# Optimization experiments

Measured on AMD Instinct MI355X. Metric: run time of the kernel, lower is better.

## Reference

```python
import jax, jax.numpy as jnp
import numpy as np

NH = 4       # num_heads
WS = 4       # window_size (in subdomains)
SHIFT = 2    # shift (in subdomains) on odd layers
SUB = 16     # physical subdomain size (y and x)
L = 4        # num_layers
EPS = 1e-5   # InstanceNorm2d eps


def _pw_mlp(x, W1, b1, W2, b2):
    # pointwise (1x1 conv) MLP over channel dim of [..., C, y, x]
    h = jnp.einsum('oc,...cyx->...oyx', W1, x) + b1[:, None, None]
    h = jax.nn.gelu(h, approximate=False)
    return jnp.einsum('oc,...cyx->...oyx', W2, h) + b2[:, None, None]


def _inorm(x):
    # InstanceNorm2d (affine=False): normalize each channel over spatial dims
    mu = jnp.mean(x, axis=(-2, -1), keepdims=True)
    var = jnp.var(x, axis=(-2, -1), keepdims=True)
    return (x - mu) * jax.lax.rsqrt(var + EPS)


def _grid_to_win(g, B, nwy, nwx):
    # g: [B, n_sub_y, n_sub_x, C, sh, sw] -> [B*nwy*nwx, WS*WS, C, sh, sw]
    C, sh, sw = g.shape[3:]
    g = g.reshape(B, nwy, WS, nwx, WS, C, sh, sw).transpose(0, 1, 3, 2, 4, 5, 6, 7)
    return g.reshape(B * nwy * nwx, WS * WS, C, sh, sw)


def _win_to_grid(d, B, nwy, nwx):
    # inverse of _grid_to_win
    C, sh, sw = d.shape[2:]
    g = d.reshape(B, nwy, nwx, WS, WS, C, sh, sw).transpose(0, 1, 3, 2, 4, 5, 6, 7)
    return g.reshape(B, nwy * WS, nwx * WS, C, sh, sw)


def _attn(d, Wq, bq, Wk, bk, Wv, bv, Wo, bo, shift, B, nwy, nwx):
    # function-space windowed self-attention; tokens are subdomain functions
    if shift > 0:
        g = _win_to_grid(d, B, nwy, nwx)
        g = jnp.roll(g, (-shift, -shift), axis=(1, 2))
        d = _grid_to_win(g, B, nwy, nwx)
    E = Wq.shape[0]
    dh = E // NH
    Bw, S, C, sh, sw = d.shape

    def proj(W, b):
        p = jnp.einsum('dc,bscyx->bsdyx', W, d) + b[:, None, None]
        return p.reshape(Bw, S, NH, dh, sh, sw)

    q, k, vv = proj(Wq, bq), proj(Wk, bk), proj(Wv, bv)
    # integral inner-product score: mean over subdomain points, / sqrt(dh)
    scale = 1.0 / ((sh * sw) * (float(dh) ** 0.5))
    scores = jnp.einsum('bihcyx,bjhcyx->bhij', q, k) * scale
    A = jax.nn.softmax(scores, axis=-1)
    o = jnp.einsum('bhij,bjhcyx->bihcyx', A, vv).reshape(Bw, S, E, sh, sw)
    o = jnp.einsum('dc,bscyx->bsdyx', Wo, o) + bo[:, None, None]
    if shift > 0:
        g = _win_to_grid(o, B, nwy, nwx)
        g = jnp.roll(g, (shift, shift), axis=(1, 2))
        o = _grid_to_win(g, B, nwy, nwx)
    return o


def _forward(v, inp_W1, inp_b1, inp_W2, inp_b2, Wq, bq, Wk, bk, Wv, bv, Wo, bo,
             mlp_W1, mlp_b1, mlp_W2, mlp_b2, out_W1, out_b1, out_W2, out_b2,
             dsy, dsx):
    B, Cin, H, W = v.shape
    n_sub_y, n_sub_x = dsy // SUB, dsx // SUB
    sh, sw = H // n_sub_y, W // n_sub_x
    nwy, nwx = n_sub_y // WS, n_sub_x // WS
    # cell-centered grid, channels (y, x)
    yc = (jnp.arange(H, dtype=v.dtype) + 0.5) * (dsy / H)
    xc = (jnp.arange(W, dtype=v.dtype) + 0.5) * (dsx / W)
    g = jnp.stack(jnp.meshgrid(yc, xc, indexing='ij'), axis=0)  # [2,H,W]
    g = jnp.broadcast_to(g, (B, 2, H, W))
    v = jnp.concatenate([g, v], axis=1)
    v = _pw_mlp(v, inp_W1, inp_b1, inp_W2, inp_b2)  # [B,E,H,W]
    E = v.shape[1]
    # win_decompose2d: pixels -> subdomain grid -> windows of WSxWS subdomains
    sgrid = v.reshape(B, E, n_sub_y, sh, n_sub_x, sw).transpose(0, 2, 4, 1, 3, 5)
    d = _grid_to_win(sgrid, B, nwy, nwx)  # [B*nw, WS*WS, E, sh, sw]
    for i in range(L):
        shift = 0 if i % 2 == 0 else SHIFT
        d = _attn(_inorm(d), Wq[i], bq[i], Wk[i], bk[i], Wv[i], bv[i],
                  Wo[i], bo[i], shift, B, nwy, nwx) + d
        d = _pw_mlp(_inorm(d), mlp_W1[i], mlp_b1[i], mlp_W2[i], mlp_b2[i]) + d
    # win_recompose2d
    sgrid = _win_to_grid(d, B, nwy, nwx)  # [B, n_sub_y, n_sub_x, E, sh, sw]
    u = sgrid.transpose(0, 3, 1, 4, 2, 5).reshape(B, E, H, W)
    return _pw_mlp(u, out_W1, out_b1, out_W2, out_b2)


def setup_inputs() -> dict:
    key = jax.random.key(0)
    ks = jax.random.split(key, 16)
    B, Cin, H, W, E, HID, Cout = 8, 3, 256, 256, 64, 128, 1
    s = 0.02
    r = lambda k, shape: (s * jax.random.normal(k, shape)).astype(jnp.float32)
    z = lambda shape: jnp.zeros(shape, jnp.float32)
    return {
        'v': jax.random.normal(ks[0], (B, Cin, H, W), dtype=jnp.float32),
        'inp_W1': r(ks[1], (HID, Cin + 2)), 'inp_b1': z((HID,)),
        'inp_W2': r(ks[2], (E, HID)), 'inp_b2': z((E,)),
        'Wq': r(ks[3], (L, E, E)), 'bq': z((L, E)),
        'Wk': r(ks[4], (L, E, E)), 'bk': z((L, E)),
        'Wv': r(ks[5], (L, E, E)), 'bv': z((L, E)),
        'Wo': r(ks[6], (L, E, E)), 'bo': z((L, E)),
        'mlp_W1': r(ks[7], (L, E, E)), 'mlp_b1': z((L, E)),
        'mlp_W2': r(ks[8], (L, E, E)), 'mlp_b2': z((L, E)),
        'out_W1': r(ks[9], (HID, E)), 'out_b1': z((HID,)),
        'out_W2': r(ks[10], (Cout, HID)), 'out_b2': z((Cout,)),
        'domain_size_y': 256, 'domain_size_x': 256,
    }


def reference(v, inp_W1, inp_b1, inp_W2, inp_b2, Wq, bq, Wk, bk, Wv, bv, Wo, bo,
              mlp_W1, mlp_b1, mlp_W2, mlp_b2, out_W1, out_b1, out_W2, out_b2,
              domain_size_y, domain_size_x):
    return _forward(v, inp_W1, inp_b1, inp_W2, inp_b2, Wq, bq, Wk, bk, Wv, bv,
                    Wo, bo, mlp_W1, mlp_b1, mlp_W2, mlp_b2, out_W1, out_b1,
                    out_W2, out_b2, domain_size_y, domain_size_x)
```

## Files before the change

### kernel.cpp

```cpp
#include <hip/hip_runtime.h>
#include <math.h>

typedef unsigned short u16;
typedef unsigned int   u32;
typedef __attribute__((ext_vector_type(8))) short bf16x8;
typedef __attribute__((ext_vector_type(4))) float f32x4;

#define NTOK  2048
#define TOKSZ 16384ull

#define CBAR() __asm__ __volatile__("" ::: "memory")

__device__ __forceinline__ float bf2f(u16 b) { return __uint_as_float(((u32)b) << 16); }
__device__ __forceinline__ u16 f2bf(float f) {
    u32 u = __float_as_uint(f);
    u += 0x7FFFu + ((u >> 16) & 1u);
    return (u16)(u >> 16);
}
__device__ __forceinline__ float gelu_f(float x) {
    return 0.5f * x * (1.0f + erff(x * 0.70710678118654752440f));
}
__device__ __forceinline__ int shift_tok(int n) {
    int w = n >> 4, s = n & 15;
    int b = w >> 4, wy = (w >> 2) & 3, wx = w & 3;
    int ty = s >> 2, tx = s & 3;
    int gy = ((wy << 2) + ty + 2) & 15;
    int gx = ((wx << 2) + tx + 2) & 15;
    int w2 = (b << 4) + ((gy >> 2) << 2) + (gx >> 2);
    int s2 = ((gy & 3) << 2) + (gx & 3);
    return (w2 << 4) + s2;
}
__device__ __forceinline__ int swz(int row, int chunk) {
    return row * 64 + ((chunk ^ (row & 7)) << 3);
}

union U8 { uint4 u; bf16x8 b; };

__global__ void detect_kernel(const u16* __restrict__ w1, int* __restrict__ flag) {
    int t = threadIdx.x, bad = 0;
    for (int i = t; i < 640; i += 64) {
        float ax = fabsf(bf2f(w1[i]));
        if (!(ax < 1e3f)) bad = 1;
    }
    unsigned long long m = __ballot(bad);
    if (t == 0) *flag = (m != 0ull) ? 1 : 0;
}

#define NWT 20
struct WArgs { const void* src[NWT]; int off16[NWT + 1]; int f32o[NWT]; };

__global__ __launch_bounds__(256)
void cvt_weights(WArgs a, const int* __restrict__ flag,
                 float* __restrict__ wbufA, u16* __restrict__ wbuf16) {
    int t = blockIdx.x * 256 + threadIdx.x;
    if (t >= a.off16[NWT]) return;
    int s = 0;
    while (a.off16[s + 1] <= t) ++s;
    int idx = t - a.off16[s];
    u16 raw; float v;
    if (*flag) { v = ((const float*)a.src[s])[idx]; raw = f2bf(v); }
    else       { raw = ((const u16*)a.src[s])[idx]; v = bf2f(raw); }
    wbuf16[t] = raw;
    if (a.f32o[s] >= 0) wbufA[a.f32o[s] + idx] = v;
}

__global__ __launch_bounds__(256, 3)
void embed_mfma(const void* __restrict__ vin, const int* __restrict__ flag,
                const float* __restrict__ W1, const float* __restrict__ b1,
                const u16* __restrict__ W2bf, const float* __restrict__ b2,
                const int* __restrict__ pdsy, const int* __restrict__ pdsx,
                float* __restrict__ d, float* __restrict__ mursg) {
    extern __shared__ char smem[];
    u16* hsT = (u16*)smem;
    u16* wl  = (u16*)(smem + 32768);
    int n = blockIdx.x, t = threadIdx.x;
    int wv = t >> 6, l = t & 63, m = l & 15, qd = l >> 4;
    int px0 = wv * 64;

    int w = n >> 4, s = n & 15;
    int b = w >> 4, wy = (w >> 2) & 3, wx = w & 3;
    int ty = s >> 2, tx = s & 3;
    int y = ((wy << 2) + ty) * 16 + (t >> 4);
    int x = ((wx << 2) + tx) * 16 + (t & 15);
    int fl = *flag;
    float in0 = ((float)y + 0.5f) * ((float)pdsy[0] * (1.0f / 256.0f));
    float in1 = ((float)x + 0.5f) * ((float)pdsx[0] * (1.0f / 256.0f));
    size_t pix = (size_t)b * 3 * 65536 + (size_t)y * 256 + (size_t)x;
    float in2 = fl ? ((const float*)vin)[pix]          : bf2f(((const u16*)vin)[pix]);
    float in3 = fl ? ((const float*)vin)[pix + 65536]  : bf2f(((const u16*)vin)[pix + 65536]);
    float in4 = fl ? ((const float*)vin)[pix + 131072] : bf2f(((const u16*)vin)[pix + 131072]);

    f32x4 acc[4][4];
    #pragma unroll
    for (int nt = 0; nt < 4; ++nt) {
        float bb = b2[nt * 16 + m];
        #pragma unroll
        for (int mt = 0; mt < 4; ++mt) acc[mt][nt] = {bb, bb, bb, bb};
    }
    for (int half = 0; half < 2; ++half) {
        if (half) __syncthreads();
        for (int h2 = 0; h2 < 64; h2 += 2) {
            int hid = half * 64 + h2;
            float ha = b1[hid] + W1[hid*5]*in0 + W1[hid*5+1]*in1 + W1[hid*5+2]*in2
                     + W1[hid*5+3]*in3 + W1[hid*5+4]*in4;
            float hb2 = b1[hid+1] + W1[hid*5+5]*in0 + W1[hid*5+6]*in1 + W1[hid*5+7]*in2
                     + W1[hid*5+8]*in3 + W1[hid*5+9]*in4;
            u32 pk = (u32)f2bf(gelu_f(ha)) | ((u32)f2bf(gelu_f(hb2)) << 16);
            *(u32*)&hsT[swz(t, h2 >> 3) + (h2 & 7)] = pk;
        }
        #pragma unroll
        for (int r = 0; r < 2; ++r) {
            int u = t + r * 256; int e = u >> 3, c8 = u & 7;
            *(uint4*)&wl[swz(e, c8)] = *(const uint4*)(W2bf + e * 128 + half * 64 + c8 * 8);
        }
        __syncthreads();
        #pragma unroll
        for (int ks = 0; ks < 2; ++ks) {
            U8 af[4], bf[4];
            #pragma unroll
            for (int mt = 0; mt < 4; ++mt)
                af[mt].u = *(const uint4*)&hsT[swz(px0 + mt*16 + m, ks*4 + qd)];
            #pragma unroll
            for (int nt = 0; nt < 4; ++nt)
                bf[nt].u = *(const uint4*)&wl[swz(nt*16 + m, ks*4 + qd)];
            #pragma unroll
            for (int mt = 0; mt < 4; ++mt)
                #pragma unroll
                for (int nt = 0; nt < 4; ++nt)
                    acc[mt][nt] = __builtin_amdgcn_mfma_f32_16x16x32_bf16(
                        af[mt].b, bf[nt].b, acc[mt][nt], 0, 0, 0);
        }
    }
    __syncthreads();
    float sv[4], qv[4];
    #pragma unroll
    for (int nt = 0; nt < 4; ++nt) {
        float ss = 0.f, qq = 0.f;
        #pragma unroll
        for (int mt = 0; mt < 4; ++mt)
            #pragma unroll
            for (int r = 0; r < 4; ++r) { float xx = acc[mt][nt][r]; ss += xx; qq = fmaf(xx, xx, qq); }
        ss += __shfl_xor(ss, 16); ss += __shfl_xor(ss, 32);
        qq += __shfl_xor(qq, 16); qq += __shfl_xor(qq, 32);
        sv[nt] = ss; qv[nt] = qq;
    }
    float* sarr = (float*)smem;
    if (qd == 0) {
        #pragma unroll
        for (int nt = 0; nt < 4; ++nt) {
            sarr[(nt*16 + m)*4 + wv] = sv[nt];
            sarr[256 + (nt*16 + m)*4 + wv] = qv[nt];
        }
    }
    __syncthreads();
    if (t < 64) {
        float ss = sarr[t*4] + sarr[t*4+1] + sarr[t*4+2] + sarr[t*4+3];
        float qq = sarr[256+t*4] + sarr[256+t*4+1] + sarr[256+t*4+2] + sarr[256+t*4+3];
        float mu = ss * (1.0f/256.0f);
        float var = qq * (1.0f/256.0f) - mu * mu;
        mursg[(size_t)n * 128 + t] = mu;
        mursg[(size_t)n * 128 + 64 + t] = rsqrtf(var + 1e-5f);
    }
    __syncthreads();
    float* eps = (float*)smem + wv * 2304;
    float* dp = d + (size_t)n * TOKSZ;
    #pragma unroll
    for (int ch2 = 0; ch2 < 2; ++ch2) {
        if (ch2) CBAR();
        #pragma unroll
        for (int mt = ch2*2; mt < ch2*2+2; ++mt)
            #pragma unroll
            for (int nt = 0; nt < 4; ++nt)
                #pragma unroll
                for (int r = 0; r < 4; ++r)
                    eps[((mt&1)*16 + qd*4 + r) * 68 + nt*16 + m] = acc[mt][nt][r];
        CBAR();
        #pragma unroll
        for (int j = 0; j < 8; ++j) {
            int f = l + 64*j; int row = f >> 4, c4 = f & 15;
            float4 v = *(float4*)&eps[row * 68 + c4 * 4];
            *(float4*)&dp[(px0 + ch2*32 + row) * 64 + c4 * 4] = v;
        }
    }
}

__device__ __forceinline__ void gemm64(const u16* xs, const u16* wl, const float* bv4,
                                       int px0, int m, int qd, u16* dst) {
    f32x4 acc[4][4];
    #pragma unroll
    for (int nt = 0; nt < 4; ++nt) {
        float bb = bv4[nt];
        #pragma unroll
        for (int mt = 0; mt < 4; ++mt) acc[mt][nt] = {bb, bb, bb, bb};
    }
    #pragma unroll
    for (int ks = 0; ks < 2; ++ks) {
        U8 af[4], bfr[4];
        #pragma unroll
        for (int mt = 0; mt < 4; ++mt)
            af[mt].u = *(const uint4*)&xs[swz(px0 + mt*16 + m, ks*4 + qd)];
        #pragma unroll
        for (int nt = 0; nt < 4; ++nt)
            bfr[nt].u = *(const uint4*)&wl[swz(nt*16 + m, ks*4 + qd)];
        #pragma unroll
        for (int mt = 0; mt < 4; ++mt)
            #pragma unroll
            for (int nt = 0; nt < 4; ++nt)
                acc[mt][nt] = __builtin_amdgcn_mfma_f32_16x16x32_bf16(
                    af[mt].b, bfr[nt].b, acc[mt][nt], 0, 0, 0);
    }
    #pragma unroll
    for (int mt = 0; mt < 4; ++mt)
        #pragma unroll
        for (int nt = 0; nt < 4; ++nt)
            #pragma unroll
            for (int r = 0; r < 4; ++r) {
                int R = px0 + mt*16 + qd*4 + r, ch = nt*16 + m;
                dst[swz(R, ch >> 3) + (ch & 7)] = f2bf(acc[mt][nt][r]);
            }
}

__global__ __launch_bounds__(256, 1)
void scores_qkv(const float* __restrict__ dres, const float* __restrict__ mursg,
                const u16* __restrict__ Wq, const float* __restrict__ bq,
                const u16* __restrict__ Wk, const float* __restrict__ bk,
                const u16* __restrict__ Wv, const float* __restrict__ bv,
                int shifted, float* __restrict__ Ap, u16* __restrict__ vbuf) {
    extern __shared__ char smem[];
    u16* xs  = (u16*)smem;
    u16* qls = (u16*)(smem + 32768);
    u16* kls = (u16*)(smem + 65536);
    u16* wlq = (u16*)(smem + 98304);
    u16* wlk = (u16*)(smem + 106496);
    u16* wlv = (u16*)(smem + 114688);
    int* nis = (int*)(smem + 122880);
    float* mloc = (float*)(smem + 122944);
    int w = blockIdx.x, half = blockIdx.y, t = threadIdx.x;
    int wv = t >> 6, l = t & 63, m = l & 15, qd = l >> 4;
    int px0 = wv * 64;
    if (t < 16) { int nn = w * 16 + t; nis[t] = shifted ? shift_tok(nn) : nn; }
    __syncthreads();
    #pragma unroll
    for (int r = 0; r < 2; ++r) {
        int u = t + r * 256; int e = u >> 3, c8 = u & 7;
        *(uint4*)&wlq[swz(e, c8)] = *(const uint4*)(Wq + e * 64 + c8 * 8);
        *(uint4*)&wlk[swz(e, c8)] = *(const uint4*)(Wk + e * 64 + c8 * 8);
        *(uint4*)&wlv[swz(e, c8)] = *(const uint4*)(Wv + e * 64 + c8 * 8);
    }
    #pragma unroll
    for (int r = 0; r < 8; ++r) {
        int u = t + r * 256;
        mloc[u] = mursg[(size_t)nis[u >> 7] * 128 + (u & 127)];
    }
    float bqv[4], bkv[4], bvv[4];
    #pragma unroll
    for (int nt = 0; nt < 4; ++nt) {
        bqv[nt] = bq[nt*16 + m]; bkv[nt] = bk[nt*16 + m]; bvv[nt] = bv[nt*16 + m];
    }
    f32x4 sacc = {0.f, 0.f, 0.f, 0.f};
    __syncthreads();
    for (int ch = 0; ch < 8; ++ch) {
        int pxb = half * 128 + ch * 16;
        #pragma unroll
        for (int i8 = 0; i8 < 8; ++i8) {
            int u = t + i8 * 256; int row = u >> 3, c8 = u & 7;
            int tok = row >> 4, pxl = row & 15;
            const float4* gp = (const float4*)
                (dres + (size_t)nis[tok] * TOKSZ + (size_t)(pxb + pxl) * 64 + c8 * 8);
            float4 f0 = gp[0], f1 = gp[1];
            const float4* mp = (const float4*)&mloc[tok * 128 + c8 * 8];
            float4 mu0 = mp[0], mu1 = mp[1];
            const float4* rp = (const float4*)&mloc[tok * 128 + 64 + c8 * 8];
            float4 rs0 = rp[0], rs1 = rp[1];
            uint4 o;
            o.x = (u32)f2bf((f0.x-mu0.x)*rs0.x) | ((u32)f2bf((f0.y-mu0.y)*rs0.y) << 16);
            o.y = (u32)f2bf((f0.z-mu0.z)*rs0.z) | ((u32)f2bf((f0.w-mu0.w)*rs0.w) << 16);
            o.z = (u32)f2bf((f1.x-mu1.x)*rs1.x) | ((u32)f2bf((f1.y-mu1.y)*rs1.y) << 16);
            o.w = (u32)f2bf((f1.z-mu1.z)*rs1.z) | ((u32)f2bf((f1.w-mu1.w)*rs1.w) << 16);
            *(uint4*)&xs[swz(row, c8)] = o;
        }
        __syncthreads();
        gemm64(xs, wlq, bqv, px0, m, qd, qls);
        gemm64(xs, wlk, bkv, px0, m, qd, kls);
        gemm64(xs, wlv, bvv, px0, m, qd, xs);
        __syncthreads();
        #pragma unroll
        for (int p2 = 0; p2 < 8; ++p2) {
            U8 af, bfr;
            int row = m * 16 + p2 * 2 + (qd >> 1);
            int c8 = wv * 2 + (qd & 1);
            af.u  = *(const uint4*)&qls[swz(row, c8)];
            bfr.u = *(const uint4*)&kls[swz(row, c8)];
            sacc = __builtin_amdgcn_mfma_f32_16x16x32_bf16(af.b, bfr.b, sacc, 0, 0, 0);
        }
        #pragma unroll
        for (int i8 = 0; i8 < 8; ++i8) {
            int u = t + i8 * 256; int row = u >> 3, c8 = u & 7;
            int tok = row >> 4, pxl = row & 15;
            *(uint4*)(vbuf + (size_t)nis[tok] * 16384 + (size_t)(pxb + pxl) * 64 + c8 * 8)
                = *(const uint4*)&xs[swz(row, c8)];
        }
        __syncthreads();
    }
    float* ap = Ap + (size_t)half * 131072 + ((size_t)w * 4 + wv) * 256;
    #pragma unroll
    for (int r = 0; r < 4; ++r)
        ap[(qd * 4 + r) * 16 + m] = sacc[r] * (1.0f / 1024.0f);
}

__global__ __launch_bounds__(256, 2)
void wo_mlp(const u16* __restrict__ vb, const float* __restrict__ Ap,
            const u16* __restrict__ Wo, const float* __restrict__ bo,
            const u16* __restrict__ W1, const float* __restrict__ b1,
            const u16* __restrict__ W2, const float* __restrict__ b2,
            int shifted, float* __restrict__ dres, float* __restrict__ mursg,
            int wmu) {
    extern __shared__ char smem[];
    u16* xs = (u16*)smem;
    u16* wl = (u16*)(smem + 32768);
    float* As = (float*)(smem + 32768);
    int*  nis = (int*)(smem + 33792);
    float* sarr = (float*)(smem + 32768);
    float* murs2 = (float*)smem;
    int bid = blockIdx.x;
    int qg = bid >> 7, r7 = bid & 127;
    int n = ((qg << 3) + (r7 & 7)) * 16 + (r7 >> 3);
    int t = threadIdx.x;
    int wv = t >> 6, l = t & 63, m = l & 15, qd = l >> 4;
    int px0 = wv * 64;
    int w = n >> 4, i = n & 15;
    int no = shifted ? shift_tok(n) : n;
    int rbase = l >> 4, c4l = l & 15;
    if (t < 16) { int nn = w * 16 + t; nis[t] = shifted ? shift_tok(nn) : nn; }
    if (t >= 64 && t < 128) {
        int u = t - 64; int h = u >> 4, j = u & 15;
        size_t ai = ((size_t)(w * 4 + h)) * 256 + i * 16 + j;
        float sc = (Ap[ai] + Ap[131072 + ai]) * (1.0f / 1024.0f);
        float mx = sc;
        #pragma unroll
        for (int off = 1; off < 16; off <<= 1) mx = fmaxf(mx, __shfl_xor(mx, off, 16));
        float e = expf(sc - mx);
        float ssum = e;
        #pragma unroll
        for (int off = 1; off < 16; off <<= 1) ssum += __shfl_xor(ssum, off, 16);
        As[u] = e / ssum;
    }
    __syncthreads();
    #pragma unroll
    for (int r = 0; r < 8; ++r) {
        int idx = r * 256 + t;
        int px = idx >> 3, c8 = idx & 7, h = c8 >> 1;
        float a0=0,a1=0,a2=0,a3=0,a4=0,a5=0,a6=0,a7=0;
        #pragma unroll
        for (int j = 0; j < 16; ++j) {
            const u16* src = vb + (size_t)nis[j] * 16384 + (size_t)px * 64 + c8 * 8;
            uint4 pv = *(const uint4*)src;
            float aw = As[h * 16 + j];
            a0 = fmaf(aw, __uint_as_float(pv.x << 16), a0);
            a1 = fmaf(aw, __uint_as_float(pv.x & 0xFFFF0000u), a1);
            a2 = fmaf(aw, __uint_as_float(pv.y << 16), a2);
            a3 = fmaf(aw, __uint_as_float(pv.y & 0xFFFF0000u), a3);
            a4 = fmaf(aw, __uint_as_float(pv.z << 16), a4);
            a5 = fmaf(aw, __uint_as_float(pv.z & 0xFFFF0000u), a5);
            a6 = fmaf(aw, __uint_as_float(pv.w << 16), a6);
            a7 = fmaf(aw, __uint_as_float(pv.w & 0xFFFF0000u), a7);
        }
        uint4 o;
        o.x = (u32)f2bf(a0) | ((u32)f2bf(a1) << 16);
        o.y = (u32)f2bf(a2) | ((u32)f2bf(a3) << 16);
        o.z = (u32)f2bf(a4) | ((u32)f2bf(a5) << 16);
        o.w = (u32)f2bf(a6) | ((u32)f2bf(a7) << 16);
        *(uint4*)&xs[swz(px, c8)] = o;
    }
    __syncthreads();
    #pragma unroll
    for (int r = 0; r < 2; ++r) {
        int u = t + r * 256;
        int e = u >> 3, c8 = u & 7;
        *(uint4*)&wl[swz(e, c8)] = *(const uint4*)(Wo + e * 64 + c8 * 8);
    }
    __syncthreads();
    f32x4 acc[4][4];
    #pragma unroll
    for (int nt = 0; nt < 4; ++nt) {
        float bb = bo[nt * 16 + m];
        #pragma unroll
        for (int mt = 0; mt < 4; ++mt) acc[mt][nt] = {bb, bb, bb, bb};
    }
    #pragma unroll
    for (int ks = 0; ks < 2; ++ks) {
        U8 af[4], bf[4];
        #pragma unroll
        for (int mt = 0; mt < 4; ++mt)
            af[mt].u = *(const uint4*)&xs[swz(px0 + mt*16 + m, ks*4 + qd)];
        #pragma unroll
        for (int nt = 0; nt < 4; ++nt)
            bf[nt].u = *(const uint4*)&wl[swz(nt*16 + m, ks*4 + qd)];
        #pragma unroll
        for (int mt = 0; mt < 4; ++mt)
            #pragma unroll
            for (int nt = 0; nt < 4; ++nt)
                acc[mt][nt] = __builtin_amdgcn_mfma_f32_16x16x32_bf16(
                    af[mt].b, bf[nt].b, acc[mt][nt], 0, 0, 0);
    }
    __syncthreads();
    float* eps = (float*)smem + wv * 2304;
    float* dp = dres + (size_t)no * TOKSZ;
    float4 xv[2][8];
    #pragma unroll
    for (int ch2 = 0; ch2 < 2; ++ch2) {
        if (ch2) CBAR();
        #pragma unroll
        for (int mt = ch2*2; mt < ch2*2+2; ++mt)
            #pragma unroll
            for (int nt = 0; nt < 4; ++nt)
                #pragma unroll
                for (int r = 0; r < 4; ++r)
                    eps[((mt&1)*16 + qd*4 + r) * 68 + nt*16 + m] = acc[mt][nt][r];
        CBAR();
        #pragma unroll
        for (int j = 0; j < 8; ++j) {
            int row = rbase + 4*j;
            float4 dv = *(float4*)&eps[row * 68 + c4l * 4];
            float4 gv = *(const float4*)&dp[(px0 + ch2*32 + row) * 64 + c4l * 4];
            gv.x += dv.x; gv.y += dv.y; gv.z += dv.z; gv.w += dv.w;
            xv[ch2][j] = gv;
        }
    }
    __syncthreads();
    float s0=0,s1=0,s2=0,s3=0,q0=0,q1=0,q2=0,q3=0;
    #pragma unroll
    for (int ch2 = 0; ch2 < 2; ++ch2)
        #pragma unroll
        for (int j = 0; j < 8; ++j) {
            float4 v = xv[ch2][j];
            s0 += v.x; q0 = fmaf(v.x, v.x, q0);
            s1 += v.y; q1 = fmaf(v.y, v.y, q1);
            s2 += v.z; q2 = fmaf(v.z, v.z, q2);
            s3 += v.w; q3 = fmaf(v.w, v.w, q3);
        }
    int cb = 4 * c4l, g = t >> 4;
    float* qarr = sarr + 1024;
    sarr[(cb+0)*16+g]=s0; sarr[(cb+1)*16+g]=s1; sarr[(cb+2)*16+g]=s2; sarr[(cb+3)*16+g]=s3;
    qarr[(cb+0)*16+g]=q0; qarr[(cb+1)*16+g]=q1; qarr[(cb+2)*16+g]=q2; qarr[(cb+3)*16+g]=q3;
    __syncthreads();
    if (t < 64) {
        float ss = 0.f, qq = 0.f;
        #pragma unroll
        for (int gg = 0; gg < 16; ++gg) { ss += sarr[t*16+gg]; qq += qarr[t*16+gg]; }
        float mu = ss * (1.0f/256.0f);
        float var = qq * (1.0f/256.0f) - mu * mu;
        murs2[t] = mu; murs2[64 + t] = rsqrtf(var + 1e-5f);
    }
    __syncthreads();
    float m0 = murs2[cb], m1 = murs2[cb+1], m2 = murs2[cb+2], m3 = murs2[cb+3];
    float r0 = murs2[64+cb], r1 = murs2[64+cb+1], r2 = murs2[64+cb+2], r3 = murs2[64+cb+3];
    __syncthreads();
    #pragma unroll
    for (int ch2 = 0; ch2 < 2; ++ch2)
        #pragma unroll
        for (int j = 0; j < 8; ++j) {
            float4 v = xv[ch2][j];
            int row = px0 + ch2*32 + rbase + 4*j;
            uint2 o;
            o.x = (u32)f2bf((v.x-m0)*r0) | ((u32)f2bf((v.y-m1)*r1) << 16);
            o.y = (u32)f2bf((v.z-m2)*r2) | ((u32)f2bf((v.w-m3)*r3) << 16);
            *(uint2*)&xs[swz(row, c4l >> 1) + (c4l & 1) * 4] = o;
        }
    #pragma unroll
    for (int r = 0; r < 2; ++r) {
        int u = t + r * 256;
        int e = u >> 3, c8 = u & 7;
        *(uint4*)&wl[swz(e, c8)] = *(const uint4*)(W1 + e * 64 + c8 * 8);
    }
    __syncthreads();
    #pragma unroll
    for (int nt = 0; nt < 4; ++nt) {
        float bb = b1[nt * 16 + m];
        #pragma unroll
        for (int mt = 0; mt < 4; ++mt) acc[mt][nt] = {bb, bb, bb, bb};
    }
    #pragma unroll
    for (int ks = 0; ks < 2; ++ks) {
        U8 af[4], bf[4];
        #pragma unroll
        for (int mt = 0; mt < 4; ++mt)
            af[mt].u = *(const uint4*)&xs[swz(px0 + mt*16 + m, ks*4 + qd)];
        #pragma unroll
        for (int nt = 0; nt < 4; ++nt)
            bf[nt].u = *(const uint4*)&wl[swz(nt*16 + m, ks*4 + qd)];
        #pragma unroll
        for (int mt = 0; mt < 4; ++mt)
            #pragma unroll
            for (int nt = 0; nt < 4; ++nt)
                acc[mt][nt] = __builtin_amdgcn_mfma_f32_16x16x32_bf16(
                    af[mt].b, bf[nt].b, acc[mt][nt], 0, 0, 0);
    }
    __syncthreads();
    #pragma unroll
    for (int nt = 0; nt < 4; ++nt) {
        int ch = nt * 16 + m;
        #pragma unroll
        for (int mt = 0; mt < 4; ++mt)
            #pragma unroll
            for (int r = 0; r < 4; ++r) {
                int R = px0 + mt*16 + qd*4 + r;
                xs[swz(R, ch >> 3) + (ch & 7)] = f2bf(gelu_f(acc[mt][nt][r]));
            }
    }
    #pragma unroll
    for (int r = 0; r < 2; ++r) {
        int u = t + r * 256;
        int e = u >> 3, c8 = u & 7;
        *(uint4*)&wl[swz(e, c8)] = *(const uint4*)(W2 + e * 64 + c8 * 8);
    }
    __syncthreads();
    #pragma unroll
    for (int nt = 0; nt < 4; ++nt) {
        float bb = b2[nt * 16 + m];
        #pragma unroll
        for (int mt = 0; mt < 4; ++mt) acc[mt][nt] = {bb, bb, bb, bb};
    }
    #pragma unroll
    for (int ks = 0; ks < 2; ++ks) {
        U8 af[4], bf[4];
        #pragma unroll
        for (int mt = 0; mt < 4; ++mt)
            af[mt].u = *(const uint4*)&xs[swz(px0 + mt*16 + m, ks*4 + qd)];
        #pragma unroll
        for (int nt = 0; nt < 4; ++nt)
            bf[nt].u = *(const uint4*)&wl[swz(nt*16 + m, ks*4 + qd)];
        #pragma unroll
        for (int mt = 0; mt < 4; ++mt)
            #pragma unroll
            for (int nt = 0; nt < 4; ++nt)
                acc[mt][nt] = __builtin_amdgcn_mfma_f32_16x16x32_bf16(
                    af[mt].b, bf[nt].b, acc[mt][nt], 0, 0, 0);
    }
    __syncthreads();
    #pragma unroll
    for (int ch2 = 0; ch2 < 2; ++ch2) {
        if (ch2) CBAR();
        #pragma unroll
        for (int mt = ch2*2; mt < ch2*2+2; ++mt)
            #pragma unroll
            for (int nt = 0; nt < 4; ++nt)
                #pragma unroll
                for (int r = 0; r < 4; ++r)
                    eps[((mt&1)*16 + qd*4 + r) * 68 + nt*16 + m] = acc[mt][nt][r];
        CBAR();
        #pragma unroll
        for (int j = 0; j < 8; ++j) {
            int row = rbase + 4*j;
            float4 dv = *(float4*)&eps[row * 68 + c4l * 4];
            float4 bs = xv[ch2][j];
            bs.x += dv.x; bs.y += dv.y; bs.z += dv.z; bs.w += dv.w;
            xv[ch2][j] = bs;
            *(float4*)&dp[(px0 + ch2*32 + row) * 64 + c4l * 4] = bs;
        }
    }
    if (wmu) {
        __syncthreads();
        float t0=0,t1=0,t2=0,t3=0,u0=0,u1=0,u2=0,u3=0;
        #pragma unroll
        for (int ch2 = 0; ch2 < 2; ++ch2)
            #pragma unroll
            for (int j = 0; j < 8; ++j) {
                float4 v = xv[ch2][j];
                t0 += v.x; u0 = fmaf(v.x, v.x, u0);
                t1 += v.y; u1 = fmaf(v.y, v.y, u1);
                t2 += v.z; u2 = fmaf(v.z, v.z, u2);
                t3 += v.w; u3 = fmaf(v.w, v.w, u3);
            }
        sarr[(cb+0)*16+g]=t0; sarr[(cb+1)*16+g]=t1; sarr[(cb+2)*16+g]=t2; sarr[(cb+3)*16+g]=t3;
        qarr[(cb+0)*16+g]=u0; qarr[(cb+1)*16+g]=u1; qarr[(cb+2)*16+g]=u2; qarr[(cb+3)*16+g]=u3;
        __syncthreads();
        if (t < 64) {
            float ss = 0.f, qq = 0.f;
            #pragma unroll
            for (int gg = 0; gg < 16; ++gg) { ss += sarr[t*16+gg]; qq += qarr[t*16+gg]; }
            float mu = ss * (1.0f/256.0f);
            float var = qq * (1.0f/256.0f) - mu * mu;
            mursg[(size_t)no * 128 + t] = mu;
            mursg[(size_t)no * 128 + 64 + t] = rsqrtf(var + 1e-5f);
        }
    }
}

__global__ __launch_bounds__(256, 3)
void wo_av(const u16* __restrict__ vb, const float* __restrict__ Ap,
           const u16* __restrict__ Wo, const float* __restrict__ bo,
           int shifted, float* __restrict__ dres) {
    extern __shared__ char smem[];
    u16* xs = (u16*)smem;
    u16* wl = (u16*)(smem + 32768);
    float* As = (float*)(smem + 40960);
    int*  nis = (int*)(smem + 41216);
    int bid = blockIdx.x;
    int qg = bid >> 7, r7 = bid & 127;
    int n = ((qg << 3) + (r7 & 7)) * 16 + (r7 >> 3);
    int t = threadIdx.x;
    int wv = t >> 6, l = t & 63, m = l & 15, qd = l >> 4;
    int px0 = wv * 64;
    int w = n >> 4, i = n & 15;
    int no = shifted ? shift_tok(n) : n;
    if (t < 16) { int nn = w * 16 + t; nis[t] = shifted ? shift_tok(nn) : nn; }
    if (t >= 64 && t < 128) {
        int u = t - 64; int h = u >> 4, j = u & 15;
        size_t ai = ((size_t)(w * 4 + h)) * 256 + i * 16 + j;
        float sc = (Ap[ai] + Ap[131072 + ai]) * (1.0f / 1024.0f);
        float mx = sc;
        #pragma unroll
        for (int off = 1; off < 16; off <<= 1) mx = fmaxf(mx, __shfl_xor(mx, off, 16));
        float e = expf(sc - mx);
        float ssum = e;
        #pragma unroll
        for (int off = 1; off < 16; off <<= 1) ssum += __shfl_xor(ssum, off, 16);
        As[u] = e / ssum;
    }
    #pragma unroll
    for (int r = 0; r < 2; ++r) {
        int u = t + r * 256;
        int e = u >> 3, c8 = u & 7;
        *(uint4*)&wl[swz(e, c8)] = *(const uint4*)(Wo + e * 64 + c8 * 8);
    }
    __syncthreads();
    #pragma unroll
    for (int r = 0; r < 8; ++r) {
        int idx = r * 256 + t;
        int px = idx >> 3, c8 = idx & 7, h = c8 >> 1;
        float a0=0,a1=0,a2=0,a3=0,a4=0,a5=0,a6=0,a7=0;
        #pragma unroll
        for (int j = 0; j < 16; ++j) {
            const u16* src = vb + (size_t)nis[j] * 16384 + (size_t)px * 64 + c8 * 8;
            uint4 pv = *(const uint4*)src;
            float aw = As[h * 16 + j];
            a0 = fmaf(aw, __uint_as_float(pv.x << 16), a0);
            a1 = fmaf(aw, __uint_as_float(pv.x & 0xFFFF0000u), a1);
            a2 = fmaf(aw, __uint_as_float(pv.y << 16), a2);
            a3 = fmaf(aw, __uint_as_float(pv.y & 0xFFFF0000u), a3);
            a4 = fmaf(aw, __uint_as_float(pv.z << 16), a4);
            a5 = fmaf(aw, __uint_as_float(pv.z & 0xFFFF0000u), a5);
            a6 = fmaf(aw, __uint_as_float(pv.w << 16), a6);
            a7 = fmaf(aw, __uint_as_float(pv.w & 0xFFFF0000u), a7);
        }
        uint4 o;
        o.x = (u32)f2bf(a0) | ((u32)f2bf(a1) << 16);
        o.y = (u32)f2bf(a2) | ((u32)f2bf(a3) << 16);
        o.z = (u32)f2bf(a4) | ((u32)f2bf(a5) << 16);
        o.w = (u32)f2bf(a6) | ((u32)f2bf(a7) << 16);
        *(uint4*)&xs[swz(px, c8)] = o;
    }
    __syncthreads();
    f32x4 acc[4][4];
    #pragma unroll
    for (int nt = 0; nt < 4; ++nt) {
        float bb = bo[nt * 16 + m];
        #pragma unroll
        for (int mt = 0; mt < 4; ++mt) acc[mt][nt] = {bb, bb, bb, bb};
    }
    #pragma unroll
    for (int ks = 0; ks < 2; ++ks) {
        U8 af[4], bf[4];
        #pragma unroll
        for (int mt = 0; mt < 4; ++mt)
            af[mt].u = *(const uint4*)&xs[swz(px0 + mt*16 + m, ks*4 + qd)];
        #pragma unroll
        for (int nt = 0; nt < 4; ++nt)
            bf[nt].u = *(const uint4*)&wl[swz(nt*16 + m, ks*4 + qd)];
        #pragma unroll
        for (int mt = 0; mt < 4; ++mt)
            #pragma unroll
            for (int nt = 0; nt < 4; ++nt)
                acc[mt][nt] = __builtin_amdgcn_mfma_f32_16x16x32_bf16(
                    af[mt].b, bf[nt].b, acc[mt][nt], 0, 0, 0);
    }
    __syncthreads();
    float* eps = (float*)smem + wv * 2304;
    float* dp = dres + (size_t)no * TOKSZ;
    #pragma unroll
    for (int ch2 = 0; ch2 < 2; ++ch2) {
        if (ch2) CBAR();
        #pragma unroll
        for (int mt = ch2*2; mt < ch2*2+2; ++mt)
            #pragma unroll
            for (int nt = 0; nt < 4; ++nt)
                #pragma unroll
                for (int r = 0; r < 4; ++r)
                    eps[((mt&1)*16 + qd*4 + r) * 68 + nt*16 + m] = acc[mt][nt][r];
        CBAR();
        #pragma unroll
        for (int j = 0; j < 8; ++j) {
            int f = l + 64*j; int row = f >> 4, c4 = f & 15;
            float4 dv = *(float4*)&eps[row * 68 + c4 * 4];
            float* gp = &dp[(px0 + ch2*32 + row) * 64 + c4 * 4];
            float4 gv = *(float4*)gp;
            gv.x += dv.x; gv.y += dv.y; gv.z += dv.z; gv.w += dv.w;
            *(float4*)gp = gv;
        }
    }
}

__global__ __launch_bounds__(256, 2)
void mlp_out(const float* __restrict__ dres,
             const u16* __restrict__ W1, const float* __restrict__ b1,
             const u16* __restrict__ W2, const float* __restrict__ b2,
             const u16* __restrict__ oW1, const float* __restrict__ ob1,
             const float* __restrict__ oW2, const float* __restrict__ ob2,
             void* __restrict__ outp, const int* __restrict__ flag) {
    extern __shared__ char smem[];
    u16* xs = (u16*)smem;
    u16* wl = (u16*)(smem + 32768);
    float* sarr = (float*)(smem + 32768);
    float* murs = (float*)smem;
    int n = blockIdx.x, t = threadIdx.x;
    int wv = t >> 6, l = t & 63, m = l & 15, qd = l >> 4;
    int px0 = wv * 64;
    int rbase = l >> 4, c4 = l & 15;
    const float4* gin = (const float4*)(dres + (size_t)n * TOKSZ);
    float4 xv[2][8];
    float s0=0,s1=0,s2=0,s3=0,q0=0,q1=0,q2=0,q3=0;
    #pragma unroll
    for (int ch2 = 0; ch2 < 2; ++ch2)
        #pragma unroll
        for (int j = 0; j < 8; ++j) {
            float4 v = gin[(px0 + ch2*32 + rbase + 4*j) * 16 + c4];
            xv[ch2][j] = v;
            s0 += v.x; q0 = fmaf(v.x, v.x, q0);
            s1 += v.y; q1 = fmaf(v.y, v.y, q1);
            s2 += v.z; q2 = fmaf(v.z, v.z, q2);
            s3 += v.w; q3 = fmaf(v.w, v.w, q3);
        }
    int cb = 4 * c4, g = t >> 4;
    sarr[(cb+0)*16+g]=s0; sarr[(cb+1)*16+g]=s1; sarr[(cb+2)*16+g]=s2; sarr[(cb+3)*16+g]=s3;
    float* qarr = sarr + 1024;
    qarr[(cb+0)*16+g]=q0; qarr[(cb+1)*16+g]=q1; qarr[(cb+2)*16+g]=q2; qarr[(cb+3)*16+g]=q3;
    __syncthreads();
    if (t < 64) {
        float ss = 0.f, qq = 0.f;
        #pragma unroll
        for (int gg = 0; gg < 16; ++gg) { ss += sarr[t*16+gg]; qq += qarr[t*16+gg]; }
        float mu = ss * (1.0f/256.0f);
        float var = qq * (1.0f/256.0f) - mu * mu;
        murs[t] = mu; murs[64 + t] = rsqrtf(var + 1e-5f);
    }
    __syncthreads();
    float m0 = murs[cb], m1 = murs[cb+1], m2 = murs[cb+2], m3 = murs[cb+3];
    float r0 = murs[64+cb], r1 = murs[64+cb+1], r2 = murs[64+cb+2], r3 = murs[64+cb+3];
    __syncthreads();
    #pragma unroll
    for (int ch2 = 0; ch2 < 2; ++ch2)
        #pragma unroll
        for (int j = 0; j < 8; ++j) {
            float4 v = xv[ch2][j];
            int row = px0 + ch2*32 + rbase + 4*j;
            uint2 o;
            o.x = (u32)f2bf((v.x-m0)*r0) | ((u32)f2bf((v.y-m1)*r1) << 16);
            o.y = (u32)f2bf((v.z-m2)*r2) | ((u32)f2bf((v.w-m3)*r3) << 16);
            *(uint2*)&xs[swz(row, c4 >> 1) + (c4 & 1) * 4] = o;
        }
    #pragma unroll
    for (int r = 0; r < 2; ++r) {
        int u = t + r * 256;
        int e = u >> 3, c8 = u & 7;
        *(uint4*)&wl[swz(e, c8)] = *(const uint4*)(W1 + e * 64 + c8 * 8);
    }
    __syncthreads();
    f32x4 acc[4][4];
    #pragma unroll
    for (int nt = 0; nt < 4; ++nt) {
        float bb = b1[nt * 16 + m];
        #pragma unroll
        for (int mt = 0; mt < 4; ++mt) acc[mt][nt] = {bb, bb, bb, bb};
    }
    #pragma unroll
    for (int ks = 0; ks < 2; ++ks) {
        U8 af[4], bf[4];
        #pragma unroll
        for (int mt = 0; mt < 4; ++mt)
            af[mt].u = *(const uint4*)&xs[swz(px0 + mt*16 + m, ks*4 + qd)];
        #pragma unroll
        for (int nt = 0; nt < 4; ++nt)
            bf[nt].u = *(const uint4*)&wl[swz(nt*16 + m, ks*4 + qd)];
        #pragma unroll
        for (int mt = 0; mt < 4; ++mt)
            #pragma unroll
            for (int nt = 0; nt < 4; ++nt)
                acc[mt][nt] = __builtin_amdgcn_mfma_f32_16x16x32_bf16(
                    af[mt].b, bf[nt].b, acc[mt][nt], 0, 0, 0);
    }
    __syncthreads();
    #pragma unroll
    for (int nt = 0; nt < 4; ++nt) {
        int ch = nt * 16 + m;
        #pragma unroll
        for (int mt = 0; mt < 4; ++mt)
            #pragma unroll
            for (int r = 0; r < 4; ++r) {
                int R = px0 + mt*16 + qd*4 + r;
                xs[swz(R, ch >> 3) + (ch & 7)] = f2bf(gelu_f(acc[mt][nt][r]));
            }
    }
    #pragma unroll
    for (int r = 0; r < 2; ++r) {
        int u = t + r * 256;
        int e = u >> 3, c8 = u & 7;
        *(uint4*)&wl[swz(e, c8)] = *(const uint4*)(W2 + e * 64 + c8 * 8);
    }
    __syncthreads();
    #pragma unroll
    for (int nt = 0; nt < 4; ++nt) {
        float bb = b2[nt * 16 + m];
        #pragma unroll
        for (int mt = 0; mt < 4; ++mt) acc[mt][nt] = {bb, bb, bb, bb};
    }
    #pragma unroll
    for (int ks = 0; ks < 2; ++ks) {
        U8 af[4], bf[4];
        #pragma unroll
        for (int mt = 0; mt < 4; ++mt)
            af[mt].u = *(const uint4*)&xs[swz(px0 + mt*16 + m, ks*4 + qd)];
        #pragma unroll
        for (int nt = 0; nt < 4; ++nt)
            bf[nt].u = *(const uint4*)&wl[swz(nt*16 + m, ks*4 + qd)];
        #pragma unroll
        for (int mt = 0; mt < 4; ++mt)
            #pragma unroll
            for (int nt = 0; nt < 4; ++nt)
                acc[mt][nt] = __builtin_amdgcn_mfma_f32_16x16x32_bf16(
                    af[mt].b, bf[nt].b, acc[mt][nt], 0, 0, 0);
    }
    __syncthreads();
    float* eps = (float*)smem + wv * 2304;
    #pragma unroll
    for (int ch2 = 0; ch2 < 2; ++ch2) {
        if (ch2) CBAR();
        #pragma unroll
        for (int mt = ch2*2; mt < ch2*2+2; ++mt)
            #pragma unroll
            for (int nt = 0; nt < 4; ++nt)
                #pragma unroll
                for (int r = 0; r < 4; ++r)
                    eps[((mt&1)*16 + qd*4 + r) * 68 + nt*16 + m] = acc[mt][nt][r];
        CBAR();
        #pragma unroll
        for (int j = 0; j < 8; ++j) {
            int row = rbase + 4*j;
            float4 dv = *(float4*)&eps[row * 68 + c4 * 4];
            float4 bs = xv[ch2][j];
            bs.x += dv.x; bs.y += dv.y; bs.z += dv.z; bs.w += dv.w;
            xv[ch2][j] = bs;
        }
    }
    __syncthreads();
    #pragma unroll
    for (int ch2 = 0; ch2 < 2; ++ch2)
        #pragma unroll
        for (int j = 0; j < 8; ++j) {
            float4 v = xv[ch2][j];
            int row = px0 + ch2*32 + rbase + 4*j;
            uint2 o;
            o.x = (u32)f2bf(v.x) | ((u32)f2bf(v.y) << 16);
            o.y = (u32)f2bf(v.z) | ((u32)f2bf(v.w) << 16);
            *(uint2*)&xs[swz(row, c4 >> 1) + (c4 & 1) * 4] = o;
        }
    __syncthreads();
    float val[4][4];
    #pragma unroll
    for (int mt = 0; mt < 4; ++mt)
        #pragma unroll
        for (int r = 0; r < 4; ++r) val[mt][r] = 0.f;
    for (int nh = 0; nh < 2; ++nh) {
        if (nh) __syncthreads();
        #pragma unroll
        for (int r = 0; r < 2; ++r) {
            int u = t + r * 256;
            int e = u >> 3, c8 = u & 7;
            *(uint4*)&wl[swz(e, c8)] = *(const uint4*)(oW1 + (size_t)nh * 4096 + e * 64 + c8 * 8);
        }
        __syncthreads();
        float w2v[4];
        #pragma unroll
        for (int nt = 0; nt < 4; ++nt) w2v[nt] = oW2[nh * 64 + nt * 16 + m];
        #pragma unroll
        for (int mtp = 0; mtp < 2; ++mtp) {
            f32x4 oacc[2][4];
            #pragma unroll
            for (int nt = 0; nt < 4; ++nt) {
                float bb = ob1[nh * 64 + nt * 16 + m];
                oacc[0][nt] = {bb, bb, bb, bb};
                oacc[1][nt] = {bb, bb, bb, bb};
            }
            #pragma unroll
            for (int ks = 0; ks < 2; ++ks) {
                U8 af[2], bf[4];
                #pragma unroll
                for (int mi = 0; mi < 2; ++mi)
                    af[mi].u = *(const uint4*)&xs[swz(px0 + (2*mtp+mi)*16 + m, ks*4 + qd)];
                #pragma unroll
                for (int nt = 0; nt < 4; ++nt)
                    bf[nt].u = *(const uint4*)&wl[swz(nt*16 + m, ks*4 + qd)];
                #pragma unroll
                for (int mi = 0; mi < 2; ++mi)
                    #pragma unroll
                    for (int nt = 0; nt < 4; ++nt)
                        oacc[mi][nt] = __builtin_amdgcn_mfma_f32_16x16x32_bf16(
                            af[mi].b, bf[nt].b, oacc[mi][nt], 0, 0, 0);
            }
            #pragma unroll
            for (int mi = 0; mi < 2; ++mi)
                #pragma unroll
                for (int r = 0; r < 4; ++r) {
                    float p = 0.f;
                    #pragma unroll
                    for (int nt = 0; nt < 4; ++nt)
                        p = fmaf(gelu_f(oacc[mi][nt][r]), w2v[nt], p);
                    val[2*mtp + mi][r] += p;
                }
        }
    }
    __syncthreads();
    float* red = (float*)smem;
    #pragma unroll
    for (int mt = 0; mt < 4; ++mt)
        #pragma unroll
        for (int r = 0; r < 4; ++r)
            red[(px0 + mt*16 + qd*4 + r) * 17 + m] = val[mt][r];
    __syncthreads();
    float a = ob2[0];
    #pragma unroll
    for (int j = 0; j < 16; ++j) a += red[t * 17 + j];
    int w = n >> 4, s = n & 15;
    int b = w >> 4, wy = (w >> 2) & 3, wx = w & 3;
    int ty = s >> 2, tx = s & 3;
    int y = ((wy << 2) + ty) * 16 + (t >> 4);
    int x = ((wx << 2) + tx) * 16 + (t & 15);
    size_t oi = (size_t)b * 65536 + (size_t)y * 256 + (size_t)x;
    if (*flag) ((float*)outp)[oi] = a;
    else       ((u16*)outp)[oi] = f2bf(a);
}

extern "C" void kernel_launch(void* const* d_in, const int* in_sizes, int n_in,
                              void* d_out, int out_size, void* d_ws, size_t ws_size,
                              hipStream_t stream) {
    (void)n_in; (void)out_size; (void)ws_size;
    const int* pdsy = (const int*)d_in[21];
    const int* pdsx = (const int*)d_in[22];

    char* wsb = (char*)d_ws;
    float* bufd  = (float*)wsb;
    u16*  vbuf   = (u16*)(wsb + 134217728ull);
    float* Ap    = (float*)(wsb + 201326592ull);
    float* mursg = (float*)(wsb + 202375168ull);
    float* wbufA = (float*)(wsb + 203423744ull);
    u16* wbuf16  = (u16*)(wsb + 203434496ull);
    int* flag    = (int*)(wsb + 203669248ull);

    const int f32set[12] = {1, 2, 4, 6, 8, 10, 12, 14, 16, 18, 19, 20};
    WArgs wa;
    int off16[NWT + 1]; off16[0] = 0;
    int c32[NWT + 1];
    int fo = 0;
    for (int i = 0; i < NWT; ++i) {
        int di = i + 1;
        wa.src[i] = d_in[di];
        off16[i + 1] = off16[i] + in_sizes[di];
        wa.off16[i] = off16[i];
        int isf = 0;
        for (int j = 0; j < 12; ++j) if (f32set[j] == di) isf = 1;
        wa.f32o[i] = isf ? fo : -1;
        c32[di] = isf ? fo : -1;
        if (isf) fo += in_sizes[di];
    }
    wa.off16[NWT] = off16[NWT];

    detect_kernel<<<1, 64, 0, stream>>>((const u16*)d_in[1], flag);
    cvt_weights<<<(off16[NWT] + 255) / 256, 256, 0, stream>>>(wa, flag, wbufA, wbuf16);

    const float* f_inpW1 = wbufA + c32[1];
    const float* f_inpb1 = wbufA + c32[2];
    const float* f_inpb2 = wbufA + c32[4];
    const float* f_bq  = wbufA + c32[6];
    const float* f_bk  = wbufA + c32[8];
    const float* f_bv  = wbufA + c32[10];
    const float* f_bo  = wbufA + c32[12];
    const float* f_mb1 = wbufA + c32[14];
    const float* f_mb2 = wbufA + c32[16];
    const float* f_ob1 = wbufA + c32[18];
    const float* f_oW2 = wbufA + c32[19];
    const float* f_ob2 = wbufA + c32[20];
    const u16* h_inpW2 = wbuf16 + off16[2];
    const u16* h_Wq  = wbuf16 + off16[4];
    const u16* h_Wk  = wbuf16 + off16[6];
    const u16* h_Wv  = wbuf16 + off16[8];
    const u16* h_Wo  = wbuf16 + off16[10];
    const u16* h_mW1 = wbuf16 + off16[12];
    const u16* h_mW2 = wbuf16 + off16[14];
    const u16* h_oW1 = wbuf16 + off16[16];

    embed_mfma<<<NTOK, 256, 40960, stream>>>(d_in[0], flag, f_inpW1, f_inpb1,
                                             h_inpW2, f_inpb2, pdsy, pdsx,
                                             bufd, mursg);

    for (int l = 0; l < 4; ++l) {
        int sh = l & 1;
        const u16* Wql = h_Wq + l * 4096;  const float* bql = f_bq + l * 64;
        const u16* Wkl = h_Wk + l * 4096;  const float* bkl = f_bk + l * 64;
        const u16* Wvl = h_Wv + l * 4096;  const float* bvl = f_bv + l * 64;
        const u16* Wol = h_Wo + l * 4096;  const float* bol = f_bo + l * 64;
        const u16* W1l = h_mW1 + l * 4096; const float* b1l = f_mb1 + l * 64;
        const u16* W2l = h_mW2 + l * 4096; const float* b2l = f_mb2 + l * 64;

        scores_qkv<<<dim3(128, 2), 256, 131136, stream>>>(
            bufd, mursg, Wql, bql, Wkl, bkl, Wvl, bvl, sh, Ap, vbuf);
        if (l < 3) {
            wo_mlp<<<NTOK, 256, 40960, stream>>>(vbuf, Ap, Wol, bol,
                                                 W1l, b1l, W2l, b2l,
                                                 sh, bufd, mursg, 1);
        } else {
            wo_av<<<NTOK, 256, 41280, stream>>>(vbuf, Ap, Wol, bol, sh, bufd);
            mlp_out<<<NTOK, 256, 40960, stream>>>(bufd, W1l, b1l, W2l, b2l,
                                                  h_oW1, f_ob1, f_oW2, f_ob2,
                                                  d_out, flag);
        }
    }
}
```

Baseline: 1.001 ms.

## Halve scores_qkv pixel chunk to cut LDS and allow two blocks per CU

The scores_qkv kernel now processes 8 pixels per token per chunk instead of 16, over 16 iterations instead of 8. This halves the LDS staging buffers and the per-wave GEMM accumulators, and the launch bound is raised to 2 blocks per CU with about 80KB of shared memory. The token index table in LDS is replaced by per-thread precomputed shifted indices. With only 256 blocks, the goal is more latency hiding per CU, at the cost of twice as many barriers and loop iterations.

```diff
diff --git a/kernel.cpp b/kernel.cpp
--- a/kernel.cpp
+++ b/kernel.cpp
@@ -184,43 +184,43 @@
     }
 }
 
-__device__ __forceinline__ void gemm64(const u16* xs, const u16* wl, const float* bv4,
-                                       int px0, int m, int qd, u16* dst) {
-    f32x4 acc[4][4];
+__device__ __forceinline__ void gemm64h(const u16* xs, const u16* wl, const float* bv4,
+                                        int px0w, int m, int qd, u16* dst) {
+    f32x4 acc[2][4];
     #pragma unroll
     for (int nt = 0; nt < 4; ++nt) {
         float bb = bv4[nt];
-        #pragma unroll
-        for (int mt = 0; mt < 4; ++mt) acc[mt][nt] = {bb, bb, bb, bb};
+        acc[0][nt] = {bb, bb, bb, bb};
+        acc[1][nt] = {bb, bb, bb, bb};
     }
     #pragma unroll
     for (int ks = 0; ks < 2; ++ks) {
-        U8 af[4], bfr[4];
-        #pragma unroll
-        for (int mt = 0; mt < 4; ++mt)
-            af[mt].u = *(const uint4*)&xs[swz(px0 + mt*16 + m, ks*4 + qd)];
+        U8 af[2], bfr[4];
+        #pragma unroll
+        for (int mi = 0; mi < 2; ++mi)
+            af[mi].u = *(const uint4*)&xs[swz(px0w + mi*16 + m, ks*4 + qd)];
         #pragma unroll
         for (int nt = 0; nt < 4; ++nt)
             bfr[nt].u = *(const uint4*)&wl[swz(nt*16 + m, ks*4 + qd)];
         #pragma unroll
-        for (int mt = 0; mt < 4; ++mt)
-            #pragma unroll
-            for (int nt = 0; nt < 4; ++nt)
-                acc[mt][nt] = __builtin_amdgcn_mfma_f32_16x16x32_bf16(
-                    af[mt].b, bfr[nt].b, acc[mt][nt], 0, 0, 0);
-    }
-    #pragma unroll
-    for (int mt = 0; mt < 4; ++mt)
+        for (int mi = 0; mi < 2; ++mi)
+            #pragma unroll
+            for (int nt = 0; nt < 4; ++nt)
+                acc[mi][nt] = __builtin_amdgcn_mfma_f32_16x16x32_bf16(
+                    af[mi].b, bfr[nt].b, acc[mi][nt], 0, 0, 0);
+    }
+    #pragma unroll
+    for (int mi = 0; mi < 2; ++mi)
         #pragma unroll
         for (int nt = 0; nt < 4; ++nt)
             #pragma unroll
             for (int r = 0; r < 4; ++r) {
-                int R = px0 + mt*16 + qd*4 + r, ch = nt*16 + m;
-                dst[swz(R, ch >> 3) + (ch & 7)] = f2bf(acc[mt][nt][r]);
+                int R = px0w + mi*16 + qd*4 + r, ch = nt*16 + m;
+                dst[swz(R, ch >> 3) + (ch & 7)] = f2bf(acc[mi][nt][r]);
             }
 }
 
-__global__ __launch_bounds__(256, 1)
+__global__ __launch_bounds__(256, 2)
 void scores_qkv(const float* __restrict__ dres, const float* __restrict__ mursg,
                 const u16* __restrict__ Wq, const float* __restrict__ bq,
                 const u16* __restrict__ Wk, const float* __restrict__ bk,
@@ -228,18 +228,28 @@
                 int shifted, float* __restrict__ Ap, u16* __restrict__ vbuf) {
     extern __shared__ char smem[];
     u16* xs  = (u16*)smem;
-    u16* qls = (u16*)(smem + 32768);
-    u16* kls = (u16*)(smem + 65536);
-    u16* wlq = (u16*)(smem + 98304);
-    u16* wlk = (u16*)(smem + 106496);
-    u16* wlv = (u16*)(smem + 114688);
-    int* nis = (int*)(smem + 122880);
-    float* mloc = (float*)(smem + 122944);
+    u16* qls = (u16*)(smem + 16384);
+    u16* kls = (u16*)(smem + 32768);
+    u16* wlq = (u16*)(smem + 49152);
+    u16* wlk = (u16*)(smem + 57344);
+    u16* wlv = (u16*)(smem + 65536);
+    float* mloc = (float*)(smem + 73728);
     int w = blockIdx.x, half = blockIdx.y, t = threadIdx.x;
     int wv = t >> 6, l = t & 63, m = l & 15, qd = l >> 4;
-    int px0 = wv * 64;
-    if (t < 16) { int nn = w * 16 + t; nis[t] = shifted ? shift_tok(nn) : nn; }
-    __syncthreads();
+    int px0w = wv * 32;
+    int nst[4];
+    #pragma unroll
+    for (int i8 = 0; i8 < 4; ++i8) {
+        int nn = w * 16 + (4 * i8 + wv);
+        nst[i8] = shifted ? shift_tok(nn) : nn;
+    }
+    #pragma unroll
+    for (int r = 0; r < 8; ++r) {
+        int u = t + r * 256;
+        int nn = w * 16 + (u >> 7);
+        int ni = shifted ? shift_tok(nn) : nn;
+        mloc[u] = mursg[(size_t)ni * 128 + (u & 127)];
+    }
     #pragma unroll
     for (int r = 0; r < 2; ++r) {
         int u = t + r * 256; int e = u >> 3, c8 = u & 7;
@@ -247,11 +257,6 @@
         *(uint4*)&wlk[swz(e, c8)] = *(const uint4*)(Wk + e * 64 + c8 * 8);
         *(uint4*)&wlv[swz(e, c8)] = *(const uint4*)(Wv + e * 64 + c8 * 8);
     }
-    #pragma unroll
-    for (int r = 0; r < 8; ++r) {
-        int u = t + r * 256;
-        mloc[u] = mursg[(size_t)nis[u >> 7] * 128 + (u & 127)];
-    }
     float bqv[4], bkv[4], bvv[4];
     #pragma unroll
     for (int nt = 0; nt < 4; ++nt) {
@@ -259,14 +264,15 @@
     }
     f32x4 sacc = {0.f, 0.f, 0.f, 0.f};
     __syncthreads();
-    for (int ch = 0; ch < 8; ++ch) {
-        int pxb = half * 128 + ch * 16;
-        #pragma unroll
-        for (int i8 = 0; i8 < 8; ++i8) {
+    for (int ch = 0; ch < 16; ++ch) {
+        int pxb = half * 128 + ch * 8;
+        #pragma unroll
+        for (int i8 = 0; i8 < 4; ++i8) {
             int u = t + i8 * 256; int row = u >> 3, c8 = u & 7;
-            int tok = row >> 4, pxl = row & 15;
+            int pxl = row & 7;
+            int tok = 4 * i8 + wv;
             const float4* gp = (const float4*)
-                (dres + (size_t)nis[tok] * TOKSZ + (size_t)(pxb + pxl) * 64 + c8 * 8);
+                (dres + (size_t)nst[i8] * TOKSZ + (size_t)(pxb + pxl) * 64 + c8 * 8);
             float4 f0 = gp[0], f1 = gp[1];
             const float4* mp = (const float4*)&mloc[tok * 128 + c8 * 8];
             float4 mu0 = mp[0], mu1 = mp[1];
@@ -280,24 +286,24 @@
             *(uint4*)&xs[swz(row, c8)] = o;
         }
         __syncthreads();
-        gemm64(xs, wlq, bqv, px0, m, qd, qls);
-        gemm64(xs, wlk, bkv, px0, m, qd, kls);
-        gemm64(xs, wlv, bvv, px0, m, qd, xs);
+        gemm64h(xs, wlq, bqv, px0w, m, qd, qls);
+        gemm64h(xs, wlk, bkv, px0w, m, qd, kls);
+        gemm64h(xs, wlv, bvv, px0w, m, qd, xs);
         __syncthreads();
         #pragma unroll
-        for (int p2 = 0; p2 < 8; ++p2) {
+        for (int p2 = 0; p2 < 4; ++p2) {
             U8 af, bfr;
-            int row = m * 16 + p2 * 2 + (qd >> 1);
+            int row = m * 8 + p2 * 2 + (qd >> 1);
             int c8 = wv * 2 + (qd & 1);
             af.u  = *(const uint4*)&qls[swz(row, c8)];
             bfr.u = *(const uint4*)&kls[swz(row, c8)];
             sacc = __builtin_amdgcn_mfma_f32_16x16x32_bf16(af.b, bfr.b, sacc, 0, 0, 0);
         }
         #pragma unroll
-        for (int i8 = 0; i8 < 8; ++i8) {
+        for (int i8 = 0; i8 < 4; ++i8) {
             int u = t + i8 * 256; int row = u >> 3, c8 = u & 7;
-            int tok = row >> 4, pxl = row & 15;
-            *(uint4*)(vbuf + (size_t)nis[tok] * 16384 + (size_t)(pxb + pxl) * 64 + c8 * 8)
+            int pxl = row & 7;
+            *(uint4*)(vbuf + (size_t)nst[i8] * 16384 + (size_t)(pxb + pxl) * 64 + c8 * 8)
                 = *(const uint4*)&xs[swz(row, c8)];
         }
         __syncthreads();
@@ -1011,7 +1017,7 @@
         const u16* W1l = h_mW1 + l * 4096; const float* b1l = f_mb1 + l * 64;
         const u16* W2l = h_mW2 + l * 4096; const float* b2l = f_mb2 + l * 64;
 
-        scores_qkv<<<dim3(128, 2), 256, 131136, stream>>>(
+        scores_qkv<<<dim3(128, 2), 256, 81920, stream>>>(
             bufd, mursg, Wql, bql, Wkl, bkl, Wvl, bvl, sh, Ap, vbuf);
         if (l < 3) {
             wo_mlp<<<NTOK, 256, 40960, stream>>>(vbuf, Ap, Wol, bol,
```

After: 957.6 us. -4.3%, faster.
